# Performance work log

Measured on AMD Instinct MI355X. Metric: run time of the kernel, lower is better.

## Reference

```python
import jax, jax.numpy as jnp
import numpy as np

N, C, OUT, S, NS = 8192, 256, 256, 8, 16  # points, in_planes, out_planes, share_planes, nsample
MID = OUT  # mid_planes = out_planes // 1
H = OUT // S  # linear_w bottleneck width
EPS = 1e-5


def _bn(x, g, b, m, v):
    # inference-mode BatchNorm1d over last (channel) dim
    return (x - m) * jax.lax.rsqrt(v + EPS) * g + b


def _knn_idx(p, k):
    # squared euclidean distances, (N,N); indices of k nearest (self included)
    sq = jnp.sum(p * p, axis=1)
    d = sq[:, None] + sq[None, :] - 2.0 * (p @ p.T)
    return jax.lax.top_k(-jax.lax.stop_gradient(d), k)[1]  # (N, k) int32


def setup_inputs() -> dict:
    key = jax.random.key(0)
    ks = jax.random.split(key, 24)
    g = lambda i, shape, s=0.05: jax.random.normal(ks[i], shape, jnp.float32) * s
    u = lambda i, shape: jax.random.uniform(ks[i], shape, dtype=jnp.float32)
    return {
        'p': u(0, (N, 3)),
        'x': g(1, (N, C), 1.0),
        'w_q': g(2, (C, MID)), 'b_q': jnp.zeros((MID,), jnp.float32),
        'w_k': g(3, (C, MID)), 'b_k': jnp.zeros((MID,), jnp.float32),
        'w_v': g(4, (C, OUT)), 'b_v': jnp.zeros((OUT,), jnp.float32),
        'p_w1': g(5, (3, 3), 0.5), 'p_b1': jnp.zeros((3,), jnp.float32),
        'p_bn_g': u(6, (3,)) + 0.5, 'p_bn_b': g(7, (3,), 0.1),
        'p_bn_m': g(8, (3,), 0.1), 'p_bn_v': u(9, (3,)) + 0.5,
        'p_w2': g(10, (3, OUT), 0.5), 'p_b2': jnp.zeros((OUT,), jnp.float32),
        'w_bn1_g': u(11, (MID,)) + 0.5, 'w_bn1_b': g(12, (MID,), 0.1),
        'w_bn1_m': g(13, (MID,), 0.1), 'w_bn1_v': u(14, (MID,)) + 0.5,
        'w_l1_w': g(15, (MID, H)), 'w_l1_b': jnp.zeros((H,), jnp.float32),
        'w_bn2_g': u(16, (H,)) + 0.5, 'w_bn2_b': g(17, (H,), 0.1),
        'w_bn2_m': g(18, (H,), 0.1), 'w_bn2_v': u(19, (H,)) + 0.5,
        'w_l2_w': g(20, (H, H)), 'w_l2_b': jnp.zeros((H,), jnp.float32),
    }


def reference(p, x, w_q, b_q, w_k, b_k, w_v, b_v,
              p_w1, p_b1, p_bn_g, p_bn_b, p_bn_m, p_bn_v, p_w2, p_b2,
              w_bn1_g, w_bn1_b, w_bn1_m, w_bn1_v, w_l1_w, w_l1_b,
              w_bn2_g, w_bn2_b, w_bn2_m, w_bn2_v, w_l2_w, w_l2_b):
    # PointTransformerLayer forward (single point cloud, o = [N])
    xq = x @ w_q + b_q            # (N, MID)
    xk = x @ w_k + b_k            # (N, MID)
    xv = x @ w_v + b_v            # (N, OUT)

    idx = _knn_idx(p, NS)         # (N, NS) KNN neighbor indices
    pr_xyz = p[idx] - p[:, None, :]   # (N, NS, 3) relative coords (with_xyz=True)
    xk_g = xk[idx]                # (N, NS, MID) gathered keys
    xv_g = xv[idx]                # (N, NS, OUT) gathered values

    # linear_p: Linear(3,3) -> BN -> ReLU -> Linear(3, OUT)
    pr = jax.nn.relu(_bn(pr_xyz @ p_w1 + p_b1, p_bn_g, p_bn_b, p_bn_m, p_bn_v))
    pr = pr @ p_w2 + p_b2         # (N, NS, OUT)

    # einops reduce 'n ns (i j)->n ns j' with j=MID is identity since MID==OUT
    r_qk = xk_g - xq[:, None, :] + pr   # (N, NS, MID)

    # linear_w: BN -> ReLU -> Linear(MID,H) -> BN -> ReLU -> Linear(H,H)
    w = jax.nn.relu(_bn(r_qk, w_bn1_g, w_bn1_b, w_bn1_m, w_bn1_v)) @ w_l1_w + w_l1_b
    w = jax.nn.relu(_bn(w, w_bn2_g, w_bn2_b, w_bn2_m, w_bn2_v)) @ w_l2_w + w_l2_b
    w = jax.nn.softmax(w, axis=1)       # softmax over neighbors (dim=1)

    v = (xv_g + pr).reshape(N, NS, S, H)      # 'n ns (s i) -> n ns s i'
    out = jnp.einsum('ntsi,nti->nsi', v, w)   # weighted aggregation over neighbors
    return out.reshape(N, OUT)
```

## Files before the change

kernel.cpp:

```cpp
#include <hip/hip_runtime.h>
#include <hip/hip_bf16.h>
#include <math.h>

#define N_PTS 8192
#define C_IN  256
#define OUT_C 256
#define NSAMP 16
#define H_W   32
#define EPSBN 1e-5f
#define GDIM  8
#define NCELL (GDIM * GDIM * GDIM)
#define CAPC  768
#define CAP_H 64

typedef short bf16x8 __attribute__((ext_vector_type(8)));
typedef float f32x4  __attribute__((ext_vector_type(4)));

__device__ __forceinline__ float dist2(const float4 a, const float4 b) {
  float dot = a.x * b.x + a.y * b.y + a.z * b.z;
  return a.w + b.w - 2.0f * dot;
}

__device__ __forceinline__ unsigned long long make_key(float d, int j) {
  unsigned int di = __float_as_uint(d);
  unsigned int ord = ((int)di >= 0) ? (di ^ 0x80000000u) : ~di;
  return ((unsigned long long)ord << 32) | (unsigned int)j;
}

__device__ __forceinline__ void chain_insert(unsigned long long (&ak)[16], unsigned long long key) {
  if (key < ak[0]) {
    #pragma unroll
    for (int s = 0; s < 15; ++s) {
      unsigned long long mn = ak[s] < key ? ak[s] : key;
      unsigned long long nx = ak[s + 1];
      ak[s] = nx > mn ? nx : mn;
    }
    ak[15] = ak[15] < key ? ak[15] : key;
  }
}

__device__ __forceinline__ float b2f(short s) {
  return __uint_as_float(((unsigned int)(unsigned short)s) << 16);
}
__device__ __forceinline__ short f2b(float v) {
  __hip_bfloat16 h = __float2bfloat16(v);
  short s;
  __builtin_memcpy(&s, &h, 2);
  return s;
}

__global__ __launch_bounds__(256) void prep_kernel(
    const float* __restrict__ p, const float* __restrict__ x,
    const float* __restrict__ wq, const float* __restrict__ wk, const float* __restrict__ wv,
    const float* __restrict__ bq, const float* __restrict__ bk, const float* __restrict__ bv,
    const float* __restrict__ l1w, const float* __restrict__ l2w,
    const float* __restrict__ bn1g, const float* __restrict__ bn1b,
    const float* __restrict__ bn1m, const float* __restrict__ bn1v,
    float4* __restrict__ p4, __hip_bfloat16* __restrict__ Bp, float* __restrict__ biasp,
    __hip_bfloat16* __restrict__ xb,
    __hip_bfloat16* __restrict__ l1wp, __hip_bfloat16* __restrict__ l2wp,
    float* __restrict__ sc1, float* __restrict__ of1,
    int* __restrict__ cursor, int* __restrict__ pt_cell) {
  int tid = blockIdx.x * blockDim.x + threadIdx.x;
  if (tid < 262144) {
    const float* xr = &x[(size_t)tid * 8];
    float4 xa = *(const float4*)xr;
    float4 xc = *(const float4*)(xr + 4);
    bf16x8 v;
    v[0] = f2b(xa.x); v[1] = f2b(xa.y); v[2] = f2b(xa.z); v[3] = f2b(xa.w);
    v[4] = f2b(xc.x); v[5] = f2b(xc.y); v[6] = f2b(xc.z); v[7] = f2b(xc.w);
    *(bf16x8*)&xb[(size_t)tid * 8] = v;
  }
  if (tid < 48 * 32 * 16 * 8) {
    int kj = tid & 7, n = (tid >> 3) & 15, kb = (tid >> 7) & 31, nt = tid >> 12;
    int k = kb * 8 + kj, col = nt * 16 + n;
    float v;
    if (col < 256)      v = wq[k * 256 + col];
    else if (col < 512) v = wk[k * 256 + (col - 256)];
    else                v = wv[k * 256 + (col - 512)];
    Bp[tid] = __float2bfloat16(v);
  }
  if (tid < 768) {
    biasp[tid] = tid < 256 ? bq[tid] : (tid < 512 ? bk[tid - 256] : bv[tid - 512]);
  }
  if (tid < 8192) {
    int kj = tid & 7, n = (tid >> 3) & 15, kb = (tid >> 7) & 31, nt = (tid >> 12) & 1;
    int k = kb * 8 + kj, col = nt * 16 + n;
    l1wp[tid] = __float2bfloat16(l1w[k * 32 + col]);
  }
  if (tid < 1024) {
    int kj = tid & 7, n = (tid >> 3) & 15, kb = (tid >> 7) & 3, nt = (tid >> 9) & 1;
    int k = kb * 8 + kj, col = nt * 16 + n;
    l2wp[tid] = __float2bfloat16(l2w[k * 32 + col]);
  }
  if (tid < 256) {
    float s1 = bn1g[tid] * rsqrtf(bn1v[tid] + EPSBN);
    sc1[tid] = s1;
    of1[tid] = bn1b[tid] - bn1m[tid] * s1;
  }
  if (tid < NCELL) cursor[tid] = 0;
  if (tid < N_PTS) {
    float px = p[tid * 3 + 0], py = p[tid * 3 + 1], pz = p[tid * 3 + 2];
    float sq = px * px;
    sq += py * py;
    sq += pz * pz;
    p4[tid] = make_float4(px, py, pz, sq);
    int cx = min(GDIM - 1, max(0, (int)(px * GDIM)));
    int cy = min(GDIM - 1, max(0, (int)(py * GDIM)));
    int cz = min(GDIM - 1, max(0, (int)(pz * GDIM)));
    pt_cell[tid] = (cz * GDIM + cy) * GDIM + cx;
  }
}

__global__ __launch_bounds__(512) void scatter_scan(
    const float4* __restrict__ p4, const int* __restrict__ pt_cell,
    int* __restrict__ cell_start, int* __restrict__ cursor,
    float4* __restrict__ sp4, int* __restrict__ sidx, int* __restrict__ rank) {
  __shared__ int buf[NCELL];
  const int t = threadIdx.x;
  buf[t] = 0;
  __syncthreads();
  for (int i = t; i < N_PTS; i += 512) atomicAdd(&buf[pt_cell[i]], 1);
  __syncthreads();
  for (int off = 1; off < NCELL; off <<= 1) {
    int add = (t >= off) ? buf[t - off] : 0;
    __syncthreads();
    buf[t] += add;
    __syncthreads();
  }
  if (blockIdx.x == 0) {
    cell_start[t + 1] = buf[t];
    if (t == 0) cell_start[0] = 0;
  }
  const int pid = blockIdx.x * 512 + t;
  const int c = pt_cell[pid];
  const int start = (c == 0) ? 0 : buf[c - 1];
  const int pos = start + atomicAdd(&cursor[c], 1);
  sp4[pos] = p4[pid];
  sidx[pos] = pid;
  rank[pid] = pos;
}

__global__ __launch_bounds__(256) void knn_gemm(
    const float4* __restrict__ sp4, const int* __restrict__ sidx,
    const int* __restrict__ cell_start, int* __restrict__ nbr,
    const __hip_bfloat16* __restrict__ xb, const __hip_bfloat16* __restrict__ Bp,
    const float* __restrict__ biasp, __hip_bfloat16* __restrict__ xqkv) {
  if (blockIdx.x >= NCELL * 2) {
    const int w = threadIdx.x >> 6;
    const int lane = threadIdx.x & 63;
    const int gw = (blockIdx.x - NCELL * 2) * 4 + w;
    const int m0 = (gw & 127) * 64;
    const int nt4 = (gw >> 7) * 4;
    const int n = lane & 15, q = lane >> 4;

    int o[4];
    #pragma unroll
    for (int mi = 0; mi < 4; ++mi) o[mi] = sidx[m0 + mi * 16 + n];

    f32x4 acc[4][4];
    #pragma unroll
    for (int mi = 0; mi < 4; ++mi)
      #pragma unroll
      for (int ni = 0; ni < 4; ++ni) acc[mi][ni] = (f32x4){0.f, 0.f, 0.f, 0.f};

    for (int k0 = 0; k0 < 256; k0 += 32) {
      bf16x8 af[4], bfr[4];
      #pragma unroll
      for (int mi = 0; mi < 4; ++mi)
        af[mi] = *(const bf16x8*)&xb[(size_t)o[mi] * 256 + k0 + q * 8];
      #pragma unroll
      for (int ni = 0; ni < 4; ++ni)
        bfr[ni] = *(const bf16x8*)&Bp[(size_t)(nt4 + ni) * 4096 + (k0 >> 3) * 128 + q * 128 + n * 8];
      #pragma unroll
      for (int mi = 0; mi < 4; ++mi)
        #pragma unroll
        for (int ni = 0; ni < 4; ++ni)
          acc[mi][ni] = __builtin_amdgcn_mfma_f32_16x16x32_bf16(af[mi], bfr[ni], acc[mi][ni], 0, 0, 0);
    }
    #pragma unroll
    for (int ni = 0; ni < 4; ++ni) {
      int col = (nt4 + ni) * 16 + n;
      float b = biasp[col];
      #pragma unroll
      for (int mi = 0; mi < 4; ++mi)
        #pragma unroll
        for (int r = 0; r < 4; ++r)
          xqkv[(size_t)(m0 + mi * 16 + q * 4 + r) * 768 + col] = __float2bfloat16(acc[mi][ni][r] + b);
    }
    return;
  }

  __shared__ float4 cpos[CAPC];
  __shared__ int    cidx[CAPC];
  __shared__ unsigned long long hk_s[8][CAP_H];
  __shared__ unsigned long long okey_s[8][16];
  __shared__ float tv_s[8][64];
  __shared__ int cnt_s[8];
  __shared__ int cell_s0_s[27];
  __shared__ int len_s[27];
  __shared__ int pref_s[28];
  __shared__ int nc_s, total_s;

  const int cell = blockIdx.x >> 1;
  const int sub  = blockIdx.x & 1;
  const int tid = threadIdx.x;
  const int hcx = cell & 7, hcy = (cell >> 3) & 7, hcz = cell >> 6;
  const int cs = cell_start[cell], ce = cell_start[cell + 1];

  const int ax0 = max(hcx - 1, 0), ax1 = min(hcx + 1, GDIM - 1);
  const int ay0 = max(hcy - 1, 0), ay1 = min(hcy + 1, GDIM - 1);
  const int az0 = max(hcz - 1, 0), az1 = min(hcz + 1, GDIM - 1);
  const int nx = ax1 - ax0 + 1, ny = ay1 - ay0 + 1, nz = az1 - az0 + 1;
  const int nbc = nx * ny * nz;

  if (tid < nbc) {
    int cx = ax0 + tid % nx;
    int cy = ay0 + (tid / nx) % ny;
    int cz = az0 + tid / (nx * ny);
    int cc = (cz * GDIM + cy) * GDIM + cx;
    int s0 = cell_start[cc];
    cell_s0_s[tid] = s0;
    len_s[tid] = cell_start[cc + 1] - s0;
  }
  __syncthreads();
  if (tid == 0) {
    int off = 0;
    for (int m = 0; m < nbc; ++m) { pref_s[m] = off; off += len_s[m]; }
    pref_s[nbc] = off;
    nc_s = nbc;
    total_s = off;
  }
  __syncthreads();
  const int nc = nc_s, total = total_s;

  for (int idx = tid; idx < total && idx < CAPC; idx += 256) {
    int c = 0;
    while (c + 1 < nc && pref_s[c + 1] <= idx) ++c;
    int g = cell_s0_s[c] + (idx - pref_s[c]);
    cpos[idx] = sp4[g];
    cidx[idx] = sidx[g];
  }
  __syncthreads();

  const int ptl = tid >> 5, slice = tid & 31;

  for (int p0 = cs + 8 * sub; p0 < ce; p0 += 16) {
    const int np = min(8, ce - p0);
    const bool pok = ptl < np;
    const int ld = pok ? (p0 + ptl) : cs;
    const float4 pi = sp4[ld];
    const int orig = sidx[ld];

    if (tid < 8) cnt_s[tid] = 0;
    if (tid < 128) okey_s[tid >> 4][tid & 15] = ~0ULL;
    __syncthreads();

    float t0 = 3.0e38f, t1 = 3.0e38f;
    for (int idx = slice; idx < total; idx += 32) {
      float4 q;
      if (idx < CAPC) q = cpos[idx];
      else {
        int c = 0;
        while (c + 1 < nc && pref_s[c + 1] <= idx) ++c;
        q = sp4[cell_s0_s[c] + (idx - pref_s[c])];
      }
      float d = dist2(pi, q);
      if (d < t1) {
        if (d < t0) { t1 = t0; t0 = d; } else { t1 = d; }
      }
    }
    tv_s[ptl][slice * 2]     = t0;
    tv_s[ptl][slice * 2 + 1] = t1;
    __syncthreads();

    int r0 = 0, r1 = 0;
    #pragma unroll 8
    for (int j = 0; j < 64; ++j) {
      float wv = tv_s[ptl][j];
      r0 += (wv < t0) ? 1 : 0;
      r1 += (wv < t1) ? 1 : 0;
    }
    float cand = fmaxf(r0 <= 15 ? t0 : -3.0e38f, r1 <= 15 ? t1 : -3.0e38f);
    cand = fmaxf(cand, __shfl_xor(cand, 1, 64));
    cand = fmaxf(cand, __shfl_xor(cand, 2, 64));
    cand = fmaxf(cand, __shfl_xor(cand, 4, 64));
    cand = fmaxf(cand, __shfl_xor(cand, 8, 64));
    cand = fmaxf(cand, __shfl_xor(cand, 16, 64));
    const float d16 = cand;

    if (pok) {
      for (int idx = slice; idx < total; idx += 32) {
        float4 q;
        int qi;
        if (idx < CAPC) { q = cpos[idx]; qi = cidx[idx]; }
        else {
          int c = 0;
          while (c + 1 < nc && pref_s[c + 1] <= idx) ++c;
          int g = cell_s0_s[c] + (idx - pref_s[c]);
          q = sp4[g]; qi = sidx[g];
        }
        float d = dist2(pi, q);
        if (d <= d16) {
          int pos = atomicAdd(&cnt_s[ptl], 1);
          if (pos < CAP_H) hk_s[ptl][pos] = make_key(d, qi);
        }
      }
    }
    __syncthreads();

    const int cntr = cnt_s[ptl];
    const bool overflow = cntr > CAP_H;
    const int cnt = overflow ? 0 : cntr;

    if (pok) {
      for (int i = slice; i < cnt; i += 32) {
        unsigned long long key = hk_s[ptl][i];
        int rk = 0;
        for (int j = 0; j < cnt; ++j) rk += (hk_s[ptl][j] < key) ? 1 : 0;
        if (rk < 16) okey_s[ptl][rk] = key;
      }
    }
    __syncthreads();

    if (slice == 0 && pok) {
      unsigned long long akm[16];
      if (!overflow) {
        #pragma unroll
        for (int s = 0; s < 16; ++s) akm[s] = okey_s[ptl][15 - s];
      } else {
        #pragma unroll
        for (int s = 0; s < 16; ++s) akm[s] = ~0ULL;
        for (int idx = 0; idx < total; ++idx) {
          float4 q; int qi;
          if (idx < CAPC) { q = cpos[idx]; qi = cidx[idx]; }
          else {
            int c = 0;
            while (c + 1 < nc && pref_s[c + 1] <= idx) ++c;
            int g = cell_s0_s[c] + (idx - pref_s[c]);
            q = sp4[g]; qi = sidx[g];
          }
          chain_insert(akm, make_key(dist2(pi, q), qi));
        }
      }
      float r;
      if (akm[0] == ~0ULL) {
        r = 1e9f;
      } else {
        unsigned int ord = (unsigned int)(akm[0] >> 32);
        unsigned int di = (ord & 0x80000000u) ? (ord ^ 0x80000000u) : ~ord;
        float dd = __uint_as_float(di);
        r = sqrtf(fmaxf(dd, 0.f)) * 1.001f + 1e-4f;
      }
      int lx = (int)fminf(fmaxf(floorf((pi.x - r) * GDIM), 0.f), (float)(GDIM - 1));
      int ux = (int)fminf(fmaxf(floorf((pi.x + r) * GDIM), 0.f), (float)(GDIM - 1));
      int ly = (int)fminf(fmaxf(floorf((pi.y - r) * GDIM), 0.f), (float)(GDIM - 1));
      int uy = (int)fminf(fmaxf(floorf((pi.y + r) * GDIM), 0.f), (float)(GDIM - 1));
      int lz = (int)fminf(fmaxf(floorf((pi.z - r) * GDIM), 0.f), (float)(GDIM - 1));
      int uz = (int)fminf(fmaxf(floorf((pi.z + r) * GDIM), 0.f), (float)(GDIM - 1));
      if (lx < ax0 || ux > ax1 || ly < ay0 || uy > ay1 || lz < az0 || uz > az1) {
        for (int cz = lz; cz <= uz; ++cz)
          for (int cy = ly; cy <= uy; ++cy)
            for (int cx = lx; cx <= ux; ++cx) {
              if (cx >= ax0 && cx <= ax1 && cy >= ay0 && cy <= ay1 && cz >= az0 && cz <= az1)
                continue;
              int cc = (cz * GDIM + cy) * GDIM + cx;
              int s0 = cell_start[cc], e0 = cell_start[cc + 1];
              for (int k = s0; k < e0; ++k) {
                float4 q = sp4[k];
                chain_insert(akm, make_key(dist2(pi, q), sidx[k]));
              }
            }
      }
      #pragma unroll
      for (int s = 0; s < 16; ++s) nbr[orig * NSAMP + s] = (int)(akm[s] & 0xFFFFFFFFu);
    }
    __syncthreads();
  }
}

__global__ __launch_bounds__(256) void fused_pt(
    const float4* __restrict__ sp4, const int* __restrict__ sidx, const int* __restrict__ rank,
    const __hip_bfloat16* __restrict__ xqkv, const int* __restrict__ nbr,
    const float* __restrict__ pw1, const float* __restrict__ pb1,
    const float* __restrict__ pbng, const float* __restrict__ pbnb,
    const float* __restrict__ pbnm, const float* __restrict__ pbnv,
    const float* __restrict__ pw2, const float* __restrict__ pb2,
    const float* __restrict__ sc1, const float* __restrict__ of1,
    const __hip_bfloat16* __restrict__ l1wp, const float* __restrict__ l1b,
    const float* __restrict__ bn2g, const float* __restrict__ bn2b,
    const float* __restrict__ bn2m, const float* __restrict__ bn2v,
    const __hip_bfloat16* __restrict__ l2wp, const float* __restrict__ l2b,
    float* __restrict__ out) {
  __shared__ __align__(16) __hip_bfloat16 a_s[2][NSAMP][264];
  __shared__ __align__(16) __hip_bfloat16 h1_s[2][NSAMP][40];
  __shared__ float w_s[2][NSAMP][33];
  __shared__ float q3_s[2][NSAMP][4];
  __shared__ int jn[2][NSAMP];
  __shared__ float psum[2][2][264];
  __shared__ int iorig[2];

  const int b0 = blockIdx.x * 2;
  const int tid = threadIdx.x;

  if (tid < 32) {
    int spt = tid >> 4, t = tid & 15;
    int b = b0 + spt;
    int i = sidx[b];
    if (t == 0) iorig[spt] = i;
    int j = nbr[i * NSAMP + t];
    int k = rank[j];
    jn[spt][t] = k;
    float4 pj = sp4[k];
    float4 pc = sp4[b];
    float rx = pj.x - pc.x;
    float ry = pj.y - pc.y;
    float rz = pj.z - pc.z;
    #pragma unroll
    for (int c3 = 0; c3 < 3; ++c3) {
      float t2 = rx * pw1[0 * 3 + c3] + ry * pw1[1 * 3 + c3] + rz * pw1[2 * 3 + c3] + pb1[c3];
      t2 = (t2 - pbnm[c3]) * rsqrtf(pbnv[c3] + EPSBN) * pbng[c3] + pbnb[c3];
      q3_s[spt][t][c3] = fmaxf(t2, 0.f);
    }
  }
  __syncthreads();

  const int pt = tid >> 7;
  const int t127 = tid & 127;
  const int g = t127 >> 5;
  const int cg = (t127 & 31) * 8;
  const int b = b0 + pt;

  float xqv[8], s1v[8], o1v[8], w20v[8], w21v[8], w22v[8], pb2v[8];
  {
    bf16x8 xq8 = *(const bf16x8*)&xqkv[(size_t)b * 768 + cg];
    #pragma unroll
    for (int u = 0; u < 8; ++u) {
      int c = cg + u;
      xqv[u] = b2f(xq8[u]);
      s1v[u] = sc1[c];
      o1v[u] = of1[c];
      w20v[u] = pw2[c];
      w21v[u] = pw2[256 + c];
      w22v[u] = pw2[512 + c];
      pb2v[u] = pb2[c];
    }
  }

  #pragma unroll
  for (int pass = 0; pass < 4; ++pass) {
    int t = g + pass * 4;
    int k = jn[pt][t];
    float q30 = q3_s[pt][t][0], q31 = q3_s[pt][t][1], q32 = q3_s[pt][t][2];
    bf16x8 xk8 = *(const bf16x8*)&xqkv[(size_t)k * 768 + 256 + cg];
    bf16x8 av;
    #pragma unroll
    for (int u = 0; u < 8; ++u) {
      float prv = q30 * w20v[u] + q31 * w21v[u] + q32 * w22v[u] + pb2v[u];
      float r = b2f(xk8[u]) - xqv[u] + prv;
      av[u] = f2b(fmaxf(r * s1v[u] + o1v[u], 0.f));
    }
    *(bf16x8*)&a_s[pt][t][cg] = av;
  }
  __syncthreads();

  const int w = tid >> 6;
  const int lane = tid & 63;
  const int mpt = w >> 1, hh = w & 1;
  const int nn = lane & 15, q = lane >> 4;
  {
    f32x4 acc = {0.f, 0.f, 0.f, 0.f};
    #pragma unroll
    for (int k0 = 0; k0 < 256; k0 += 32) {
      bf16x8 a = *(const bf16x8*)&a_s[mpt][nn][k0 + q * 8];
      bf16x8 bb = *(const bf16x8*)&l1wp[hh * 4096 + (k0 >> 3) * 128 + q * 128 + nn * 8];
      acc = __builtin_amdgcn_mfma_f32_16x16x32_bf16(a, bb, acc, 0, 0, 0);
    }
    int h = hh * 16 + nn;
    float s2 = bn2g[h] * rsqrtf(bn2v[h] + EPSBN);
    float o2 = bn2b[h] - bn2m[h] * s2;
    float l1bh = l1b[h];
    #pragma unroll
    for (int r = 0; r < 4; ++r)
      h1_s[mpt][q * 4 + r][h] = __float2bfloat16(fmaxf((acc[r] + l1bh) * s2 + o2, 0.f));
  }
  __syncthreads();

  {
    bf16x8 a = *(const bf16x8*)&h1_s[mpt][nn][q * 8];
    bf16x8 bb = *(const bf16x8*)&l2wp[hh * 512 + q * 128 + nn * 8];
    f32x4 z = {0.f, 0.f, 0.f, 0.f};
    f32x4 d = __builtin_amdgcn_mfma_f32_16x16x32_bf16(a, bb, z, 0, 0, 0);
    int h = hh * 16 + nn;
    float l2bh = l2b[h];
    #pragma unroll
    for (int r = 0; r < 4; ++r) w_s[mpt][q * 4 + r][h] = d[r] + l2bh;
  }
  __syncthreads();

  if (tid < 64) {
    int spt = tid >> 5, h = tid & 31;
    float m = -1e30f;
    #pragma unroll
    for (int t = 0; t < NSAMP; ++t) m = fmaxf(m, w_s[spt][t][h]);
    float e[NSAMP];
    float ssum = 0.f;
    #pragma unroll
    for (int t = 0; t < NSAMP; ++t) { e[t] = __expf(w_s[spt][t][h] - m); ssum += e[t]; }
    float inv = 1.f / ssum;
    #pragma unroll
    for (int t = 0; t < NSAMP; ++t) w_s[spt][t][h] = e[t] * inv;
  }
  __syncthreads();

  const int hb = cg & 31;
  float acc8[8];
  #pragma unroll
  for (int u = 0; u < 8; ++u) acc8[u] = 0.f;
  #pragma unroll
  for (int pass = 0; pass < 4; ++pass) {
    int t = g + pass * 4;
    int k = jn[pt][t];
    float q30 = q3_s[pt][t][0], q31 = q3_s[pt][t][1], q32 = q3_s[pt][t][2];
    bf16x8 xv8 = *(const bf16x8*)&xqkv[(size_t)k * 768 + 512 + cg];
    #pragma unroll
    for (int u = 0; u < 8; ++u) {
      float prv = q30 * w20v[u] + q31 * w21v[u] + q32 * w22v[u] + pb2v[u];
      acc8[u] += (b2f(xv8[u]) + prv) * w_s[pt][t][hb + u];
    }
  }
  #pragma unroll
  for (int u = 0; u < 8; ++u) acc8[u] += __shfl_xor(acc8[u], 32, 64);
  if ((lane >> 5) == 0) {
    #pragma unroll
    for (int u = 0; u < 8; ++u) psum[mpt][hh][cg + u] = acc8[u];
  }
  __syncthreads();
  {
    int opt = tid >> 7;
    int c0 = (tid & 127) * 2;
    float v0 = psum[opt][0][c0] + psum[opt][1][c0];
    float v1 = psum[opt][0][c0 + 1] + psum[opt][1][c0 + 1];
    int io = iorig[opt];
    *(float2*)&out[(size_t)io * OUT_C + c0] = make_float2(v0, v1);
  }
}

extern "C" void kernel_launch(void* const* d_in, const int* in_sizes, int n_in,
                              void* d_out, int out_size, void* d_ws, size_t ws_size,
                              hipStream_t stream) {
  const float* p    = (const float*)d_in[0];
  const float* x    = (const float*)d_in[1];
  const float* wq   = (const float*)d_in[2];
  const float* bq   = (const float*)d_in[3];
  const float* wk   = (const float*)d_in[4];
  const float* bk   = (const float*)d_in[5];
  const float* wv   = (const float*)d_in[6];
  const float* bv   = (const float*)d_in[7];
  const float* pw1  = (const float*)d_in[8];
  const float* pb1  = (const float*)d_in[9];
  const float* pbng = (const float*)d_in[10];
  const float* pbnb = (const float*)d_in[11];
  const float* pbnm = (const float*)d_in[12];
  const float* pbnv = (const float*)d_in[13];
  const float* pw2  = (const float*)d_in[14];
  const float* pb2  = (const float*)d_in[15];
  const float* bn1g = (const float*)d_in[16];
  const float* bn1b = (const float*)d_in[17];
  const float* bn1m = (const float*)d_in[18];
  const float* bn1v = (const float*)d_in[19];
  const float* l1w  = (const float*)d_in[20];
  const float* l1b  = (const float*)d_in[21];
  const float* bn2g = (const float*)d_in[22];
  const float* bn2b = (const float*)d_in[23];
  const float* bn2m = (const float*)d_in[24];
  const float* bn2v = (const float*)d_in[25];
  const float* l2w  = (const float*)d_in[26];
  const float* l2b  = (const float*)d_in[27];
  float* out = (float*)d_out;

  char* ws = (char*)d_ws;
  float4* p4       = (float4*)(ws + 0x000000);
  float*  biasp    = (float*)(ws + 0x040000);
  int*    cursor   = (int*)(ws + 0x042800);
  int*    cell_st  = (int*)(ws + 0x043000);
  int*    pt_cell  = (int*)(ws + 0x044000);
  float4* sp4      = (float4*)(ws + 0x050000);
  int*    sidx     = (int*)(ws + 0x070000);
  __hip_bfloat16* l1wp = (__hip_bfloat16*)(ws + 0x080000);
  __hip_bfloat16* l2wp = (__hip_bfloat16*)(ws + 0x084000);
  float*  sc1      = (float*)(ws + 0x085000);
  float*  of1      = (float*)(ws + 0x085800);
  int*    rank     = (int*)(ws + 0x088000);
  int*    nbr      = (int*)(ws + 0x090000);
  __hip_bfloat16* Bp   = (__hip_bfloat16*)(ws + 0x110000);
  __hip_bfloat16* xb   = (__hip_bfloat16*)(ws + 0x170000);
  __hip_bfloat16* xqkv = (__hip_bfloat16*)(ws + 0x570000);

  prep_kernel<<<dim3(1024), dim3(256), 0, stream>>>(
      p, x, wq, wk, wv, bq, bk, bv, l1w, l2w, bn1g, bn1b, bn1m, bn1v,
      p4, Bp, biasp, xb, l1wp, l2wp, sc1, of1, cursor, pt_cell);
  scatter_scan<<<dim3(16), dim3(512), 0, stream>>>(
      p4, pt_cell, cell_st, cursor, sp4, sidx, rank);
  knn_gemm<<<dim3(NCELL * 2 + 384), dim3(256), 0, stream>>>(
      sp4, sidx, cell_st, nbr, xb, Bp, biasp, xqkv);
  fused_pt<<<dim3(N_PTS / 2), dim3(256), 0, stream>>>(
      sp4, sidx, rank, xqkv, nbr, pw1, pb1, pbng, pbnb, pbnm, pbnv, pw2, pb2,
      sc1, of1, l1wp, l1b, bn2g, bn2b, bn2m, bn2v, l2wp, l2b, out);
}
```

Baseline: 198.3 us.

## Split KNN cells across four blocks and replace block barriers with wave-level sync

The KNN part of the fused kernel now gives each grid cell four blocks instead of two. Blocks with no points to process exit early. Per-point work inside a block is made wave-independent: the block-wide __syncthreads calls become wave barriers, shared-memory distance scans are unrolled by four, and the rank count is unrolled. The common no-overflow, no-spill case writes neighbours in parallel across 16 lanes instead of through a single lane. This cuts barrier stalls and serial tail work, at the cost of launching more blocks that each restage neighbour cells into shared memory.

```diff
diff --git a/kernel.cpp b/kernel.cpp
--- a/kernel.cpp
+++ b/kernel.cpp
@@ -12,6 +12,7 @@
 #define NCELL (GDIM * GDIM * GDIM)
 #define CAPC  768
 #define CAP_H 64
+#define NSUB  4
 
 typedef short bf16x8 __attribute__((ext_vector_type(8)));
 typedef float f32x4  __attribute__((ext_vector_type(4)));
@@ -36,6 +37,12 @@
       ak[s] = nx > mn ? nx : mn;
     }
     ak[15] = ak[15] < key ? ak[15] : key;
+  }
+}
+
+__device__ __forceinline__ void ins2(float d, float& t0, float& t1) {
+  if (d < t1) {
+    if (d < t0) { t1 = t0; t0 = d; } else { t1 = d; }
   }
 }
 
@@ -146,10 +153,10 @@
     const int* __restrict__ cell_start, int* __restrict__ nbr,
     const __hip_bfloat16* __restrict__ xb, const __hip_bfloat16* __restrict__ Bp,
     const float* __restrict__ biasp, __hip_bfloat16* __restrict__ xqkv) {
-  if (blockIdx.x >= NCELL * 2) {
+  if (blockIdx.x >= NCELL * NSUB) {
     const int w = threadIdx.x >> 6;
     const int lane = threadIdx.x & 63;
-    const int gw = (blockIdx.x - NCELL * 2) * 4 + w;
+    const int gw = (blockIdx.x - NCELL * NSUB) * 4 + w;
     const int m0 = (gw & 127) * 64;
     const int nt4 = (gw >> 7) * 4;
     const int n = lane & 15, q = lane >> 4;
@@ -191,22 +198,24 @@
     return;
   }
 
+  const int cell = blockIdx.x >> 2;
+  const int sub  = blockIdx.x & 3;
+  const int cs = cell_start[cell], ce = cell_start[cell + 1];
+  if (cs + 8 * sub >= ce) return;
+
   __shared__ float4 cpos[CAPC];
   __shared__ int    cidx[CAPC];
   __shared__ unsigned long long hk_s[8][CAP_H];
   __shared__ unsigned long long okey_s[8][16];
-  __shared__ float tv_s[8][64];
+  __shared__ float2 tv2_s[8][32];
   __shared__ int cnt_s[8];
   __shared__ int cell_s0_s[27];
   __shared__ int len_s[27];
   __shared__ int pref_s[28];
   __shared__ int nc_s, total_s;
 
-  const int cell = blockIdx.x >> 1;
-  const int sub  = blockIdx.x & 1;
   const int tid = threadIdx.x;
   const int hcx = cell & 7, hcy = (cell >> 3) & 7, hcz = cell >> 6;
-  const int cs = cell_start[cell], ce = cell_start[cell + 1];
 
   const int ax0 = max(hcx - 1, 0), ax1 = min(hcx + 1, GDIM - 1);
   const int ay0 = max(hcy - 1, 0), ay1 = min(hcy + 1, GDIM - 1);
@@ -233,8 +242,9 @@
   }
   __syncthreads();
   const int nc = nc_s, total = total_s;
-
-  for (int idx = tid; idx < total && idx < CAPC; idx += 256) {
+  const int tstage = total < CAPC ? total : CAPC;
+
+  for (int idx = tid; idx < tstage; idx += 256) {
     int c = 0;
     while (c + 1 < nc && pref_s[c + 1] <= idx) ++c;
     int g = cell_s0_s[c] + (idx - pref_s[c]);
@@ -245,120 +255,177 @@
 
   const int ptl = tid >> 5, slice = tid & 31;
 
-  for (int p0 = cs + 8 * sub; p0 < ce; p0 += 16) {
+  for (int p0 = cs + 8 * sub; p0 < ce; p0 += 8 * NSUB) {
     const int np = min(8, ce - p0);
     const bool pok = ptl < np;
-    const int ld = pok ? (p0 + ptl) : cs;
-    const float4 pi = sp4[ld];
-    const int orig = sidx[ld];
-
-    if (tid < 8) cnt_s[tid] = 0;
-    if (tid < 128) okey_s[tid >> 4][tid & 15] = ~0ULL;
-    __syncthreads();
-
-    float t0 = 3.0e38f, t1 = 3.0e38f;
-    for (int idx = slice; idx < total; idx += 32) {
-      float4 q;
-      if (idx < CAPC) q = cpos[idx];
-      else {
+    if (pok) {
+      const int ld = p0 + ptl;
+      const float4 pi = sp4[ld];
+      const int orig = sidx[ld];
+
+      if (slice == 0) cnt_s[ptl] = 0;
+      if (slice < 16) okey_s[ptl][slice] = ~0ULL;
+      hk_s[ptl][slice] = ~0ULL;
+      hk_s[ptl][slice + 32] = ~0ULL;
+      __builtin_amdgcn_wave_barrier();
+
+      float t0 = 3.0e38f, t1 = 3.0e38f;
+      int idx = slice;
+      for (; idx + 96 < tstage; idx += 128) {
+        float4 q0 = cpos[idx];
+        float4 q1 = cpos[idx + 32];
+        float4 q2 = cpos[idx + 64];
+        float4 q3 = cpos[idx + 96];
+        float d0 = dist2(pi, q0);
+        float d1 = dist2(pi, q1);
+        float d2 = dist2(pi, q2);
+        float d3 = dist2(pi, q3);
+        ins2(d0, t0, t1); ins2(d1, t0, t1); ins2(d2, t0, t1); ins2(d3, t0, t1);
+      }
+      for (; idx < tstage; idx += 32) {
+        ins2(dist2(pi, cpos[idx]), t0, t1);
+      }
+      for (; idx < total; idx += 32) {
         int c = 0;
         while (c + 1 < nc && pref_s[c + 1] <= idx) ++c;
-        q = sp4[cell_s0_s[c] + (idx - pref_s[c])];
-      }
-      float d = dist2(pi, q);
-      if (d < t1) {
-        if (d < t0) { t1 = t0; t0 = d; } else { t1 = d; }
-      }
-    }
-    tv_s[ptl][slice * 2]     = t0;
-    tv_s[ptl][slice * 2 + 1] = t1;
-    __syncthreads();
-
-    int r0 = 0, r1 = 0;
-    #pragma unroll 8
-    for (int j = 0; j < 64; ++j) {
-      float wv = tv_s[ptl][j];
-      r0 += (wv < t0) ? 1 : 0;
-      r1 += (wv < t1) ? 1 : 0;
-    }
-    float cand = fmaxf(r0 <= 15 ? t0 : -3.0e38f, r1 <= 15 ? t1 : -3.0e38f);
-    cand = fmaxf(cand, __shfl_xor(cand, 1, 64));
-    cand = fmaxf(cand, __shfl_xor(cand, 2, 64));
-    cand = fmaxf(cand, __shfl_xor(cand, 4, 64));
-    cand = fmaxf(cand, __shfl_xor(cand, 8, 64));
-    cand = fmaxf(cand, __shfl_xor(cand, 16, 64));
-    const float d16 = cand;
-
-    if (pok) {
-      for (int idx = slice; idx < total; idx += 32) {
-        float4 q;
-        int qi;
-        if (idx < CAPC) { q = cpos[idx]; qi = cidx[idx]; }
-        else {
-          int c = 0;
-          while (c + 1 < nc && pref_s[c + 1] <= idx) ++c;
-          int g = cell_s0_s[c] + (idx - pref_s[c]);
-          q = sp4[g]; qi = sidx[g];
-        }
-        float d = dist2(pi, q);
-        if (d <= d16) {
-          int pos = atomicAdd(&cnt_s[ptl], 1);
-          if (pos < CAP_H) hk_s[ptl][pos] = make_key(d, qi);
-        }
-      }
-    }
-    __syncthreads();
-
-    const int cntr = cnt_s[ptl];
-    const bool overflow = cntr > CAP_H;
-    const int cnt = overflow ? 0 : cntr;
-
-    if (pok) {
+        float4 q = sp4[cell_s0_s[c] + (idx - pref_s[c])];
+        ins2(dist2(pi, q), t0, t1);
+      }
+      tv2_s[ptl][slice] = make_float2(t0, t1);
+      __builtin_amdgcn_wave_barrier();
+
+      int r0 = 0, r1 = 0;
+      #pragma unroll 8
+      for (int j = 0; j < 32; ++j) {
+        float2 wv = tv2_s[ptl][j];
+        r0 += (wv.x < t0) ? 1 : 0;
+        r0 += (wv.y < t0) ? 1 : 0;
+        r1 += (wv.x < t1) ? 1 : 0;
+        r1 += (wv.y < t1) ? 1 : 0;
+      }
+      float cand = fmaxf(r0 <= 15 ? t0 : -3.0e38f, r1 <= 15 ? t1 : -3.0e38f);
+      cand = fmaxf(cand, __shfl_xor(cand, 1, 64));
+      cand = fmaxf(cand, __shfl_xor(cand, 2, 64));
+      cand = fmaxf(cand, __shfl_xor(cand, 4, 64));
+      cand = fmaxf(cand, __shfl_xor(cand, 8, 64));
+      cand = fmaxf(cand, __shfl_xor(cand, 16, 64));
+      const float d16 = cand;
+
+      idx = slice;
+      for (; idx + 96 < tstage; idx += 128) {
+        float4 q0 = cpos[idx];
+        float4 q1 = cpos[idx + 32];
+        float4 q2 = cpos[idx + 64];
+        float4 q3 = cpos[idx + 96];
+        int i0 = cidx[idx];
+        int i1 = cidx[idx + 32];
+        int i2 = cidx[idx + 64];
+        int i3 = cidx[idx + 96];
+        float d0 = dist2(pi, q0);
+        float d1 = dist2(pi, q1);
+        float d2 = dist2(pi, q2);
+        float d3 = dist2(pi, q3);
+        if (d0 <= d16) { int pos = atomicAdd(&cnt_s[ptl], 1); if (pos < CAP_H) hk_s[ptl][pos] = make_key(d0, i0); }
+        if (d1 <= d16) { int pos = atomicAdd(&cnt_s[ptl], 1); if (pos < CAP_H) hk_s[ptl][pos] = make_key(d1, i1); }
+        if (d2 <= d16) { int pos = atomicAdd(&cnt_s[ptl], 1); if (pos < CAP_H) hk_s[ptl][pos] = make_key(d2, i2); }
+        if (d3 <= d16) { int pos = atomicAdd(&cnt_s[ptl], 1); if (pos < CAP_H) hk_s[ptl][pos] = make_key(d3, i3); }
+      }
+      for (; idx < tstage; idx += 32) {
+        float d = dist2(pi, cpos[idx]);
+        if (d <= d16) { int pos = atomicAdd(&cnt_s[ptl], 1); if (pos < CAP_H) hk_s[ptl][pos] = make_key(d, cidx[idx]); }
+      }
+      for (; idx < total; idx += 32) {
+        int c = 0;
+        while (c + 1 < nc && pref_s[c + 1] <= idx) ++c;
+        int g = cell_s0_s[c] + (idx - pref_s[c]);
+        float d = dist2(pi, sp4[g]);
+        if (d <= d16) { int pos = atomicAdd(&cnt_s[ptl], 1); if (pos < CAP_H) hk_s[ptl][pos] = make_key(d, sidx[g]); }
+      }
+      __builtin_amdgcn_wave_barrier();
+
+      const int cntr = cnt_s[ptl];
+      const bool overflow = cntr > CAP_H;
+      const int cnt = overflow ? 0 : cntr;
+      const int cntR = (cnt + 3) & ~3;
+
       for (int i = slice; i < cnt; i += 32) {
         unsigned long long key = hk_s[ptl][i];
         int rk = 0;
-        for (int j = 0; j < cnt; ++j) rk += (hk_s[ptl][j] < key) ? 1 : 0;
+        for (int j = 0; j < cntR; j += 4) {
+          unsigned long long k0 = hk_s[ptl][j];
+          unsigned long long k1 = hk_s[ptl][j + 1];
+          unsigned long long k2 = hk_s[ptl][j + 2];
+          unsigned long long k3 = hk_s[ptl][j + 3];
+          rk += (k0 < key) ? 1 : 0;
+          rk += (k1 < key) ? 1 : 0;
+          rk += (k2 < key) ? 1 : 0;
+          rk += (k3 < key) ? 1 : 0;
+        }
         if (rk < 16) okey_s[ptl][rk] = key;
       }
-    }
-    __syncthreads();
-
-    if (slice == 0 && pok) {
-      unsigned long long akm[16];
-      if (!overflow) {
-        #pragma unroll
-        for (int s = 0; s < 16; ++s) akm[s] = okey_s[ptl][15 - s];
-      } else {
-        #pragma unroll
-        for (int s = 0; s < 16; ++s) akm[s] = ~0ULL;
-        for (int idx = 0; idx < total; ++idx) {
-          float4 q; int qi;
-          if (idx < CAPC) { q = cpos[idx]; qi = cidx[idx]; }
+      __builtin_amdgcn_wave_barrier();
+
+      unsigned long long kmax = okey_s[ptl][15];
+      bool trigger;
+      int lx, ux, ly, uy, lz, uz;
+      {
+        float r;
+        if (kmax == ~0ULL) {
+          r = 1e9f;
+        } else {
+          unsigned int ord = (unsigned int)(kmax >> 32);
+          unsigned int di = (ord & 0x80000000u) ? (ord ^ 0x80000000u) : ~ord;
+          float dd = __uint_as_float(di);
+          r = sqrtf(fmaxf(dd, 0.f)) * 1.001f + 1e-4f;
+        }
+        lx = (int)fminf(fmaxf(floorf((pi.x - r) * GDIM), 0.f), (float)(GDIM - 1));
+        ux = (int)fminf(fmaxf(floorf((pi.x + r) * GDIM), 0.f), (float)(GDIM - 1));
+        ly = (int)fminf(fmaxf(floorf((pi.y - r) * GDIM), 0.f), (float)(GDIM - 1));
+        uy = (int)fminf(fmaxf(floorf((pi.y + r) * GDIM), 0.f), (float)(GDIM - 1));
+        lz = (int)fminf(fmaxf(floorf((pi.z - r) * GDIM), 0.f), (float)(GDIM - 1));
+        uz = (int)fminf(fmaxf(floorf((pi.z + r) * GDIM), 0.f), (float)(GDIM - 1));
+        trigger = (lx < ax0 || ux > ax1 || ly < ay0 || uy > ay1 || lz < az0 || uz > az1);
+      }
+
+      if (!overflow && !trigger) {
+        if (slice < 16) {
+          unsigned long long key = okey_s[ptl][15 - slice];
+          nbr[orig * NSAMP + slice] = (int)(key & 0xFFFFFFFFu);
+        }
+      } else if (slice == 0) {
+        unsigned long long akm[16];
+        if (!overflow) {
+          #pragma unroll
+          for (int s = 0; s < 16; ++s) akm[s] = okey_s[ptl][15 - s];
+        } else {
+          #pragma unroll
+          for (int s = 0; s < 16; ++s) akm[s] = ~0ULL;
+          for (int idx2 = 0; idx2 < total; ++idx2) {
+            float4 q; int qi;
+            if (idx2 < CAPC) { q = cpos[idx2]; qi = cidx[idx2]; }
+            else {
+              int c = 0;
+              while (c + 1 < nc && pref_s[c + 1] <= idx2) ++c;
+              int g = cell_s0_s[c] + (idx2 - pref_s[c]);
+              q = sp4[g]; qi = sidx[g];
+            }
+            chain_insert(akm, make_key(dist2(pi, q), qi));
+          }
+          float r;
+          if (akm[0] == ~0ULL) r = 1e9f;
           else {
-            int c = 0;
-            while (c + 1 < nc && pref_s[c + 1] <= idx) ++c;
-            int g = cell_s0_s[c] + (idx - pref_s[c]);
-            q = sp4[g]; qi = sidx[g];
+            unsigned int ord = (unsigned int)(akm[0] >> 32);
+            unsigned int di = (ord & 0x80000000u) ? (ord ^ 0x80000000u) : ~ord;
+            float dd = __uint_as_float(di);
+            r = sqrtf(fmaxf(dd, 0.f)) * 1.001f + 1e-4f;
           }
-          chain_insert(akm, make_key(dist2(pi, q), qi));
+          lx = (int)fminf(fmaxf(floorf((pi.x - r) * GDIM), 0.f), (float)(GDIM - 1));
+          ux = (int)fminf(fmaxf(floorf((pi.x + r) * GDIM), 0.f), (float)(GDIM - 1));
+          ly = (int)fminf(fmaxf(floorf((pi.y - r) * GDIM), 0.f), (float)(GDIM - 1));
+          uy = (int)fminf(fmaxf(floorf((pi.y + r) * GDIM), 0.f), (float)(GDIM - 1));
+          lz = (int)fminf(fmaxf(floorf((pi.z - r) * GDIM), 0.f), (float)(GDIM - 1));
+          uz = (int)fminf(fmaxf(floorf((pi.z + r) * GDIM), 0.f), (float)(GDIM - 1));
         }
-      }
-      float r;
-      if (akm[0] == ~0ULL) {
-        r = 1e9f;
-      } else {
-        unsigned int ord = (unsigned int)(akm[0] >> 32);
-        unsigned int di = (ord & 0x80000000u) ? (ord ^ 0x80000000u) : ~ord;
-        float dd = __uint_as_float(di);
-        r = sqrtf(fmaxf(dd, 0.f)) * 1.001f + 1e-4f;
-      }
-      int lx = (int)fminf(fmaxf(floorf((pi.x - r) * GDIM), 0.f), (float)(GDIM - 1));
-      int ux = (int)fminf(fmaxf(floorf((pi.x + r) * GDIM), 0.f), (float)(GDIM - 1));
-      int ly = (int)fminf(fmaxf(floorf((pi.y - r) * GDIM), 0.f), (float)(GDIM - 1));
-      int uy = (int)fminf(fmaxf(floorf((pi.y + r) * GDIM), 0.f), (float)(GDIM - 1));
-      int lz = (int)fminf(fmaxf(floorf((pi.z - r) * GDIM), 0.f), (float)(GDIM - 1));
-      int uz = (int)fminf(fmaxf(floorf((pi.z + r) * GDIM), 0.f), (float)(GDIM - 1));
-      if (lx < ax0 || ux > ax1 || ly < ay0 || uy > ay1 || lz < az0 || uz > az1) {
         for (int cz = lz; cz <= uz; ++cz)
           for (int cy = ly; cy <= uy; ++cy)
             for (int cx = lx; cx <= ux; ++cx) {
@@ -371,11 +438,11 @@
                 chain_insert(akm, make_key(dist2(pi, q), sidx[k]));
               }
             }
-      }
-      #pragma unroll
-      for (int s = 0; s < 16; ++s) nbr[orig * NSAMP + s] = (int)(akm[s] & 0xFFFFFFFFu);
-    }
-    __syncthreads();
+        #pragma unroll
+        for (int s = 0; s < 16; ++s) nbr[orig * NSAMP + s] = (int)(akm[s] & 0xFFFFFFFFu);
+      }
+      __builtin_amdgcn_wave_barrier();
+    }
   }
 }
 
@@ -602,7 +669,7 @@
       p4, Bp, biasp, xb, l1wp, l2wp, sc1, of1, cursor, pt_cell);
   scatter_scan<<<dim3(16), dim3(512), 0, stream>>>(
       p4, pt_cell, cell_st, cursor, sp4, sidx, rank);
-  knn_gemm<<<dim3(NCELL * 2 + 384), dim3(256), 0, stream>>>(
+  knn_gemm<<<dim3(NCELL * NSUB + 384), dim3(256), 0, stream>>>(
       sp4, sidx, cell_st, nbr, xb, Bp, biasp, xqkv);
   fused_pt<<<dim3(N_PTS / 2), dim3(256), 0, stream>>>(
       sp4, sidx, rank, xqkv, nbr, pw1, pb1, pbng, pbnb, pbnm, pbnv, pw2, pb2,
```

Measured after the change: 216.4 us. +9.1%, slower.

## Parallelize KNN out-of-neighborhood search across lanes and reorder GEMM blocks first

Applied to the files above, without the earlier changes.

The KNN refinement previously had a single lane per point run a serial insertion-sort scan over extra cells whenever the search sphere left the 3x3x3 neighborhood. Now the sphere is computed from the threshold estimate, and all 32 lanes scan those extra cells into the shared candidate buffer. The buffer grows from 64 to 96 entries, and the final 16 indices are written in parallel. GEMM blocks are moved to the front of the grid, empty KNN blocks exit early, and the neighborhood load into shared memory is done cell by cell so the prefix search is avoided. The larger buffer raises shared memory use and may lower occupancy.

```diff
diff --git a/kernel.cpp b/kernel.cpp
--- a/kernel.cpp
+++ b/kernel.cpp
@@ -11,7 +11,8 @@
 #define GDIM  8
 #define NCELL (GDIM * GDIM * GDIM)
 #define CAPC  768
-#define CAP_H 64
+#define CAP_H 96
+#define GEMM_BLKS 384
 
 typedef short bf16x8 __attribute__((ext_vector_type(8)));
 typedef float f32x4  __attribute__((ext_vector_type(4)));
@@ -146,10 +147,10 @@
     const int* __restrict__ cell_start, int* __restrict__ nbr,
     const __hip_bfloat16* __restrict__ xb, const __hip_bfloat16* __restrict__ Bp,
     const float* __restrict__ biasp, __hip_bfloat16* __restrict__ xqkv) {
-  if (blockIdx.x >= NCELL * 2) {
+  if (blockIdx.x < GEMM_BLKS) {
     const int w = threadIdx.x >> 6;
     const int lane = threadIdx.x & 63;
-    const int gw = (blockIdx.x - NCELL * 2) * 4 + w;
+    const int gw = blockIdx.x * 4 + w;
     const int m0 = (gw & 127) * 64;
     const int nt4 = (gw >> 7) * 4;
     const int n = lane & 15, q = lane >> 4;
@@ -191,6 +192,12 @@
     return;
   }
 
+  const int kbid = blockIdx.x - GEMM_BLKS;
+  const int cell = kbid >> 1;
+  const int sub  = kbid & 1;
+  const int cs = cell_start[cell], ce = cell_start[cell + 1];
+  if (cs + 8 * sub >= ce) return;
+
   __shared__ float4 cpos[CAPC];
   __shared__ int    cidx[CAPC];
   __shared__ unsigned long long hk_s[8][CAP_H];
@@ -202,11 +209,8 @@
   __shared__ int pref_s[28];
   __shared__ int nc_s, total_s;
 
-  const int cell = blockIdx.x >> 1;
-  const int sub  = blockIdx.x & 1;
   const int tid = threadIdx.x;
   const int hcx = cell & 7, hcy = (cell >> 3) & 7, hcz = cell >> 6;
-  const int cs = cell_start[cell], ce = cell_start[cell + 1];
 
   const int ax0 = max(hcx - 1, 0), ax1 = min(hcx + 1, GDIM - 1);
   const int ay0 = max(hcy - 1, 0), ay1 = min(hcy + 1, GDIM - 1);
@@ -234,12 +238,16 @@
   __syncthreads();
   const int nc = nc_s, total = total_s;
 
-  for (int idx = tid; idx < total && idx < CAPC; idx += 256) {
-    int c = 0;
-    while (c + 1 < nc && pref_s[c + 1] <= idx) ++c;
-    int g = cell_s0_s[c] + (idx - pref_s[c]);
-    cpos[idx] = sp4[g];
-    cidx[idx] = sidx[g];
+  {
+    const int grp = tid >> 5, ln = tid & 31;
+    for (int m = grp; m < nbc; m += 8) {
+      int base = pref_s[m], src = cell_s0_s[m];
+      int lim = min(len_s[m], CAPC - base);
+      for (int i = ln; i < lim; i += 32) {
+        cpos[base + i] = sp4[src + i];
+        cidx[base + i] = sidx[src + i];
+      }
+    }
   }
   __syncthreads();
 
@@ -288,6 +296,15 @@
     cand = fmaxf(cand, __shfl_xor(cand, 8, 64));
     cand = fmaxf(cand, __shfl_xor(cand, 16, 64));
     const float d16 = cand;
+
+    const float rg = sqrtf(fmaxf(d16, 0.f)) * 1.001f + 1e-4f;
+    const int lx = (int)fminf(fmaxf(floorf((pi.x - rg) * GDIM), 0.f), (float)(GDIM - 1));
+    const int ux = (int)fminf(fmaxf(floorf((pi.x + rg) * GDIM), 0.f), (float)(GDIM - 1));
+    const int ly = (int)fminf(fmaxf(floorf((pi.y - rg) * GDIM), 0.f), (float)(GDIM - 1));
+    const int uy = (int)fminf(fmaxf(floorf((pi.y + rg) * GDIM), 0.f), (float)(GDIM - 1));
+    const int lz = (int)fminf(fmaxf(floorf((pi.z - rg) * GDIM), 0.f), (float)(GDIM - 1));
+    const int uz = (int)fminf(fmaxf(floorf((pi.z + rg) * GDIM), 0.f), (float)(GDIM - 1));
+    const bool trigger = (lx < ax0 || ux > ax1 || ly < ay0 || uy > ay1 || lz < az0 || uz > az1);
 
     if (pok) {
       for (int idx = slice; idx < total; idx += 32) {
@@ -306,59 +323,7 @@
           if (pos < CAP_H) hk_s[ptl][pos] = make_key(d, qi);
         }
       }
-    }
-    __syncthreads();
-
-    const int cntr = cnt_s[ptl];
-    const bool overflow = cntr > CAP_H;
-    const int cnt = overflow ? 0 : cntr;
-
-    if (pok) {
-      for (int i = slice; i < cnt; i += 32) {
-        unsigned long long key = hk_s[ptl][i];
-        int rk = 0;
-        for (int j = 0; j < cnt; ++j) rk += (hk_s[ptl][j] < key) ? 1 : 0;
-        if (rk < 16) okey_s[ptl][rk] = key;
-      }
-    }
-    __syncthreads();
-
-    if (slice == 0 && pok) {
-      unsigned long long akm[16];
-      if (!overflow) {
-        #pragma unroll
-        for (int s = 0; s < 16; ++s) akm[s] = okey_s[ptl][15 - s];
-      } else {
-        #pragma unroll
-        for (int s = 0; s < 16; ++s) akm[s] = ~0ULL;
-        for (int idx = 0; idx < total; ++idx) {
-          float4 q; int qi;
-          if (idx < CAPC) { q = cpos[idx]; qi = cidx[idx]; }
-          else {
-            int c = 0;
-            while (c + 1 < nc && pref_s[c + 1] <= idx) ++c;
-            int g = cell_s0_s[c] + (idx - pref_s[c]);
-            q = sp4[g]; qi = sidx[g];
-          }
-          chain_insert(akm, make_key(dist2(pi, q), qi));
-        }
-      }
-      float r;
-      if (akm[0] == ~0ULL) {
-        r = 1e9f;
-      } else {
-        unsigned int ord = (unsigned int)(akm[0] >> 32);
-        unsigned int di = (ord & 0x80000000u) ? (ord ^ 0x80000000u) : ~ord;
-        float dd = __uint_as_float(di);
-        r = sqrtf(fmaxf(dd, 0.f)) * 1.001f + 1e-4f;
-      }
-      int lx = (int)fminf(fmaxf(floorf((pi.x - r) * GDIM), 0.f), (float)(GDIM - 1));
-      int ux = (int)fminf(fmaxf(floorf((pi.x + r) * GDIM), 0.f), (float)(GDIM - 1));
-      int ly = (int)fminf(fmaxf(floorf((pi.y - r) * GDIM), 0.f), (float)(GDIM - 1));
-      int uy = (int)fminf(fmaxf(floorf((pi.y + r) * GDIM), 0.f), (float)(GDIM - 1));
-      int lz = (int)fminf(fmaxf(floorf((pi.z - r) * GDIM), 0.f), (float)(GDIM - 1));
-      int uz = (int)fminf(fmaxf(floorf((pi.z + r) * GDIM), 0.f), (float)(GDIM - 1));
-      if (lx < ax0 || ux > ax1 || ly < ay0 || uy > ay1 || lz < az0 || uz > az1) {
+      if (trigger) {
         for (int cz = lz; cz <= uz; ++cz)
           for (int cy = ly; cy <= uy; ++cy)
             for (int cx = lx; cx <= ux; ++cx) {
@@ -366,12 +331,78 @@
                 continue;
               int cc = (cz * GDIM + cy) * GDIM + cx;
               int s0 = cell_start[cc], e0 = cell_start[cc + 1];
-              for (int k = s0; k < e0; ++k) {
-                float4 q = sp4[k];
-                chain_insert(akm, make_key(dist2(pi, q), sidx[k]));
+              for (int k = s0 + slice; k < e0; k += 32) {
+                float d = dist2(pi, sp4[k]);
+                if (d <= d16) {
+                  int pos = atomicAdd(&cnt_s[ptl], 1);
+                  if (pos < CAP_H) hk_s[ptl][pos] = make_key(d, sidx[k]);
+                }
               }
             }
       }
+    }
+    __syncthreads();
+
+    const int cntr = cnt_s[ptl];
+    const bool overflow = cntr > CAP_H;
+    const int cnt = overflow ? 0 : cntr;
+
+    if (pok) {
+      for (int i = slice; i < cnt; i += 32) {
+        unsigned long long key = hk_s[ptl][i];
+        int rk = 0;
+        for (int j = 0; j < cnt; ++j) rk += (hk_s[ptl][j] < key) ? 1 : 0;
+        if (rk < 16) okey_s[ptl][rk] = key;
+      }
+    }
+    __syncthreads();
+
+    if (!overflow) {
+      if (pok && slice < 16) {
+        unsigned long long key = okey_s[ptl][15 - slice];
+        nbr[orig * NSAMP + slice] = (int)(key & 0xFFFFFFFFu);
+      }
+    } else if (pok && slice == 0) {
+      unsigned long long akm[16];
+      #pragma unroll
+      for (int s = 0; s < 16; ++s) akm[s] = ~0ULL;
+      for (int idx2 = 0; idx2 < total; ++idx2) {
+        float4 q; int qi;
+        if (idx2 < CAPC) { q = cpos[idx2]; qi = cidx[idx2]; }
+        else {
+          int c = 0;
+          while (c + 1 < nc && pref_s[c + 1] <= idx2) ++c;
+          int g = cell_s0_s[c] + (idx2 - pref_s[c]);
+          q = sp4[g]; qi = sidx[g];
+        }
+        chain_insert(akm, make_key(dist2(pi, q), qi));
+      }
+      float r;
+      if (akm[0] == ~0ULL) r = 1e9f;
+      else {
+        unsigned int ord = (unsigned int)(akm[0] >> 32);
+        unsigned int di = (ord & 0x80000000u) ? (ord ^ 0x80000000u) : ~ord;
+        float dd = __uint_as_float(di);
+        r = sqrtf(fmaxf(dd, 0.f)) * 1.001f + 1e-4f;
+      }
+      int flx = (int)fminf(fmaxf(floorf((pi.x - r) * GDIM), 0.f), (float)(GDIM - 1));
+      int fux = (int)fminf(fmaxf(floorf((pi.x + r) * GDIM), 0.f), (float)(GDIM - 1));
+      int fly = (int)fminf(fmaxf(floorf((pi.y - r) * GDIM), 0.f), (float)(GDIM - 1));
+      int fuy = (int)fminf(fmaxf(floorf((pi.y + r) * GDIM), 0.f), (float)(GDIM - 1));
+      int flz = (int)fminf(fmaxf(floorf((pi.z - r) * GDIM), 0.f), (float)(GDIM - 1));
+      int fuz = (int)fminf(fmaxf(floorf((pi.z + r) * GDIM), 0.f), (float)(GDIM - 1));
+      for (int cz = flz; cz <= fuz; ++cz)
+        for (int cy = fly; cy <= fuy; ++cy)
+          for (int cx = flx; cx <= fux; ++cx) {
+            if (cx >= ax0 && cx <= ax1 && cy >= ay0 && cy <= ay1 && cz >= az0 && cz <= az1)
+              continue;
+            int cc = (cz * GDIM + cy) * GDIM + cx;
+            int s0 = cell_start[cc], e0 = cell_start[cc + 1];
+            for (int k = s0; k < e0; ++k) {
+              float4 q = sp4[k];
+              chain_insert(akm, make_key(dist2(pi, q), sidx[k]));
+            }
+          }
       #pragma unroll
       for (int s = 0; s < 16; ++s) nbr[orig * NSAMP + s] = (int)(akm[s] & 0xFFFFFFFFu);
     }
@@ -602,7 +633,7 @@
       p4, Bp, biasp, xb, l1wp, l2wp, sc1, of1, cursor, pt_cell);
   scatter_scan<<<dim3(16), dim3(512), 0, stream>>>(
       p4, pt_cell, cell_st, cursor, sp4, sidx, rank);
-  knn_gemm<<<dim3(NCELL * 2 + 384), dim3(256), 0, stream>>>(
+  knn_gemm<<<dim3(GEMM_BLKS + NCELL * 2), dim3(256), 0, stream>>>(
       sp4, sidx, cell_st, nbr, xb, Bp, biasp, xqkv);
   fused_pt<<<dim3(N_PTS / 2), dim3(256), 0, stream>>>(
       sp4, sidx, rank, xqkv, nbr, pw1, pb1, pbng, pbnb, pbnm, pbnv, pw2, pb2,
```

After: 197.9 us. About the same (-0.2%).
